# Optimization experiments

Measured on AMD Instinct MI355X. Metric: run time of the kernel, lower is better.

Reference implementation:

```python
import jax, jax.numpy as jnp
import numpy as np

N = 100000
E = 1600000
IN_C = 128
OUT_C = 64
ALPHA = 0.2  # LeakyReLU negative slope


def _xavier(key, shape, gain=1.414):
    fan_in, fan_out = shape[-2] if len(shape) > 1 else shape[-1], shape[-1]
    bound = gain * np.sqrt(6.0 / (shape[0] * 0 + (shape[-2] if len(shape) > 1 else 1) + shape[-1])) if False else gain * np.sqrt(6.0 / (sum(shape)))
    return jax.random.uniform(key, shape, jnp.float32, -bound, bound)


def setup_inputs() -> dict:
    key = jax.random.key(0)
    k_x, k_s, k_o, k_w, k_a = jax.random.split(key, 5)
    x = jax.random.normal(k_x, (N, IN_C), jnp.float32)
    # edge list with no self-loops (so remove_self_loops is a no-op)
    src = jax.random.randint(k_s, (E,), 0, N)
    off = jax.random.randint(k_o, (E,), 1, N)
    dst = (src + off) % N
    edge_index = jnp.stack([src, dst]).astype(jnp.int64)
    W = _xavier(k_w, (IN_C, OUT_C))
    a = _xavier(k_a, (1, 2 * OUT_C))
    return {"x": x, "W": W, "a": a, "edge_index": edge_index}


def reference(x, W, a, edge_index):
    h = x @ W                               # [N, D]
    n, d = h.shape
    loops = jnp.arange(n, dtype=edge_index.dtype)
    src = jnp.concatenate([edge_index[0], loops])   # add_self_loops
    dst = jnp.concatenate([edge_index[1], loops])
    # (cat(h[src], h[dst]) * a).sum(-1) == h[src]@a1 + h[dst]@a2
    a1, a2 = a[0, :d], a[0, d:]
    s = h @ a1                              # [N]
    t = h @ a2                              # [N]
    edge_e = jnp.exp(jax.nn.leaky_relu(s[src] + t[dst], negative_slope=ALPHA))  # [E+N]
    e_expsum = jax.ops.segment_sum(edge_e, src, num_segments=n)                  # [N]
    h_prime = jax.ops.segment_sum(edge_e[:, None] * h[dst], src, num_segments=n)  # [N, D]
    return h_prime / e_expsum[:, None]
```

## Files before the change

### kernel.cpp

```cpp
#include <hip/hip_runtime.h>
#include <math.h>

#define IN_C 128
#define OUT_C 64
#define ALPHA 0.2f

#define LDK 136

#define BSH 7
#define NPB 128
#define MAXB 1024
#define PA_EPT 4
#define PA_THREADS 1024
#define PA_TILE (PA_THREADS * PA_EPT)
#define CHUNK 4096

typedef __attribute__((ext_vector_type(8))) short short8;
typedef __attribute__((ext_vector_type(4))) float v4f;

__device__ __forceinline__ ushort f2b(float f) {
  unsigned u = __float_as_uint(f);
  u += 0x7fffu + ((u >> 16) & 1u);
  return (ushort)(u >> 16);
}

__global__ __launch_bounds__(256) void gemm_st_kernel(
    const float* __restrict__ x, const float* __restrict__ W,
    const float* __restrict__ a, ushort* __restrict__ hb,
    float* __restrict__ s, float* __restrict__ t, int* __restrict__ gcur,
    int nbuck, int cape, int n_nodes, int n_tiles) {
  __shared__ ushort xs[64 * LDK];
  __shared__ ushort ws[64 * LDK];

  const int tid = threadIdx.x;
  const int wave = tid >> 6;
  const int lane = tid & 63;
  const int li = lane & 15;
  const int quad = lane >> 4;

  if (blockIdx.x == 0) {
    for (int i = tid; i < nbuck; i += 256) gcur[i] = i * cape;
  }

  for (int i = tid; i < IN_C * OUT_C; i += 256) {
    const int k = i >> 6;
    const int n = i & 63;
    ws[n * LDK + k] = f2b(W[i]);
  }
  __syncthreads();

  short8 bfrag[4][4];
#pragma unroll
  for (int ct = 0; ct < 4; ++ct)
#pragma unroll
    for (int kk = 0; kk < 4; ++kk)
      bfrag[ct][kk] =
          *(const short8*)&ws[(ct * 16 + li) * LDK + kk * 32 + quad * 8];

  float a1v[4], a2v[4];
#pragma unroll
  for (int ct = 0; ct < 4; ++ct) {
    a1v[ct] = a[ct * 16 + li];
    a2v[ct] = a[OUT_C + ct * 16 + li];
  }

  for (int tile = blockIdx.x; tile < n_tiles; tile += gridDim.x) {
    const int row0 = tile * 64;

    __syncthreads();
    for (int i = tid; i < 64 * (IN_C / 4); i += 256) {
      const int r = i >> 5;
      const int c4 = i & 31;
      int row = row0 + r;
      row = row < n_nodes ? row : n_nodes - 1;
      const float4 v = *(const float4*)&x[(size_t)row * IN_C + c4 * 4];
      uint2 p;
      p.x = (unsigned)f2b(v.x) | ((unsigned)f2b(v.y) << 16);
      p.y = (unsigned)f2b(v.z) | ((unsigned)f2b(v.w) << 16);
      *(uint2*)&xs[r * LDK + c4 * 4] = p;
    }
    __syncthreads();

    v4f acc[4];
#pragma unroll
    for (int ct = 0; ct < 4; ++ct) acc[ct] = (v4f){0.f, 0.f, 0.f, 0.f};

    const int rbase = wave * 16;
#pragma unroll
    for (int kk = 0; kk < 4; ++kk) {
      const short8 af =
          *(const short8*)&xs[(rbase + li) * LDK + kk * 32 + quad * 8];
#pragma unroll
      for (int ct = 0; ct < 4; ++ct)
        acc[ct] = __builtin_amdgcn_mfma_f32_16x16x32_bf16(af, bfrag[ct][kk],
                                                          acc[ct], 0, 0, 0);
    }

    float ps[4] = {0.f, 0.f, 0.f, 0.f};
    float pt[4] = {0.f, 0.f, 0.f, 0.f};
#pragma unroll
    for (int ct = 0; ct < 4; ++ct) {
#pragma unroll
      for (int r = 0; r < 4; ++r) {
        const float hv = acc[ct][r];
        ps[r] += hv * a1v[ct];
        pt[r] += hv * a2v[ct];
      }
    }
#pragma unroll
    for (int m = 1; m <= 8; m <<= 1) {
#pragma unroll
      for (int r = 0; r < 4; ++r) {
        ps[r] += __shfl_xor(ps[r], m, 64);
        pt[r] += __shfl_xor(pt[r], m, 64);
      }
    }
    const int growbase = row0 + rbase + quad * 4;
    if (li < 4) {
      const int grow = growbase + li;
      if (grow < n_nodes) {
        const float sv = li == 0 ? ps[0] : li == 1 ? ps[1] : li == 2 ? ps[2] : ps[3];
        const float tv = li == 0 ? pt[0] : li == 1 ? pt[1] : li == 2 ? pt[2] : pt[3];
        s[grow] = sv;
        t[grow] = tv;
      }
    }

    __syncthreads();
#pragma unroll
    for (int ct = 0; ct < 4; ++ct)
#pragma unroll
      for (int r = 0; r < 4; ++r)
        xs[(rbase + quad * 4 + r) * LDK + ct * 16 + li] = f2b(acc[ct][r]);
    __syncthreads();
    for (int j = tid; j < 64 * 8; j += 256) {
      const int row = j >> 3;
      const int u8 = j & 7;
      const int grow = row0 + row;
      if (grow < n_nodes) {
        const uint4 v = *(const uint4*)&xs[row * LDK + u8 * 8];
        *(uint4*)&hb[(size_t)grow * OUT_C + u8 * 8] = v;
      }
    }
  }
}

__global__ __launch_bounds__(PA_THREADS) void pa_bin(
    const int* __restrict__ src, const int* __restrict__ dst,
    int* __restrict__ gcur, int* __restrict__ pairs, int nbuck, int cape,
    int E) {
  __shared__ int hist[MAXB];
  __shared__ int loffs[MAXB];
  __shared__ int lcur[MAXB];
  __shared__ int gbase[MAXB];
  __shared__ int wsum[16];
  __shared__ int sl[PA_TILE];
  __shared__ ushort sbkt[PA_TILE];

  const int tid = threadIdx.x;
  const int lane = tid & 63;
  const int wid = tid >> 6;
  hist[tid] = 0;
  __syncthreads();

  const int eblk0 = blockIdx.x * PA_TILE;
  const int nblk_edges = min(PA_TILE, E - eblk0);
  const int e0 = eblk0 + tid * PA_EPT;

  int4 sv, dv;
  const bool full = (e0 + PA_EPT <= E);
  if (full) {
    sv = *(const int4*)(src + e0);
    dv = *(const int4*)(dst + e0);
    atomicAdd(&hist[sv.x >> BSH], 1);
    atomicAdd(&hist[sv.y >> BSH], 1);
    atomicAdd(&hist[sv.z >> BSH], 1);
    atomicAdd(&hist[sv.w >> BSH], 1);
  } else {
    for (int e = e0; e < E; ++e) atomicAdd(&hist[src[e] >> BSH], 1);
  }
  __syncthreads();

  const int c = hist[tid];
  gbase[tid] = c ? atomicAdd(&gcur[tid], c) : 0;

  int incl = c;
#pragma unroll
  for (int off = 1; off < 64; off <<= 1) {
    const int o = __shfl_up(incl, off, 64);
    if (lane >= off) incl += o;
  }
  if (lane == 63) wsum[wid] = incl;
  __syncthreads();
  if (tid < 16) {
    const int v = wsum[tid];
    int sc = v;
#pragma unroll
    for (int off = 1; off < 16; off <<= 1) {
      const int o = __shfl_up(sc, off, 64);
      if (tid >= off) sc += o;
    }
    wsum[tid] = sc - v;
  }
  __syncthreads();
  const int excl = incl - c + wsum[wid];
  loffs[tid] = excl;
  lcur[tid] = excl;
  __syncthreads();

#define PUTS(svv, dvv)                                        \
  {                                                           \
    const int bkt = (svv) >> BSH;                             \
    const int pos = atomicAdd(&lcur[bkt], 1);                 \
    sl[pos] = (((svv) & (NPB - 1)) << 25) | (dvv);            \
    sbkt[pos] = (ushort)bkt;                                  \
  }
  if (full) {
    PUTS(sv.x, dv.x);
    PUTS(sv.y, dv.y);
    PUTS(sv.z, dv.z);
    PUTS(sv.w, dv.w);
  } else {
    for (int e = e0; e < E; ++e) {
      const int svv = src[e];
      const int dvv = dst[e];
      PUTS(svv, dvv);
    }
  }
#undef PUTS
  __syncthreads();

  for (int k = tid; k < nblk_edges; k += PA_THREADS) {
    const int bkt = sbkt[k];
    const int gpos = gbase[bkt] + (k - loffs[bkt]);
    if (gpos < (bkt + 1) * cape) pairs[gpos] = sl[k];
  }
}

#define ACC8(o, p, wgt)                                      \
  acc[(o) + 0] += (wgt)*__uint_as_float((p).x << 16);        \
  acc[(o) + 1] += (wgt)*__uint_as_float((p).x & 0xffff0000u);\
  acc[(o) + 2] += (wgt)*__uint_as_float((p).y << 16);        \
  acc[(o) + 3] += (wgt)*__uint_as_float((p).y & 0xffff0000u);\
  acc[(o) + 4] += (wgt)*__uint_as_float((p).z << 16);        \
  acc[(o) + 5] += (wgt)*__uint_as_float((p).z & 0xffff0000u);\
  acc[(o) + 6] += (wgt)*__uint_as_float((p).w << 16);        \
  acc[(o) + 7] += (wgt)*__uint_as_float((p).w & 0xffff0000u);

__global__ __launch_bounds__(256) void aggregate_sorted(
    const int* __restrict__ pairs, const int* __restrict__ gcur,
    const uint4* __restrict__ hb4, const float* __restrict__ s,
    const float* __restrict__ t, float* __restrict__ out, int n_nodes,
    int cape) {
  __shared__ int sl[CHUNK];
  __shared__ int cnt[NPB];
  __shared__ int loffs[NPB];
  __shared__ int cur[NPB];
  __shared__ int w0tot_sh;

  const int b = blockIdx.x;
  const int tid = threadIdx.x;
  const int base = b * cape;
  int fill = gcur[b] - base;
  fill = fill < cape ? fill : cape;

  const int local = tid >> 1;
  const int half = tid & 1;
  const int u = b * NPB + local;
  const bool valid = u < n_nodes;
  const float su = valid ? s[u] : 0.f;

  float acc[32];
#pragma unroll
  for (int i = 0; i < 32; ++i) acc[i] = 0.f;
  float den = 0.f;

  for (int c0 = 0; c0 < fill; c0 += CHUNK) {
    const int clen = min(CHUNK, fill - c0);
    if (tid < NPB) cnt[tid] = 0;
    __syncthreads();

    int pw[CHUNK / 256];
#pragma unroll
    for (int j = 0; j < CHUNK / 256; ++j) {
      const int k = j * 256 + tid;
      if (k < clen) {
        pw[j] = pairs[base + c0 + k];
        atomicAdd(&cnt[((unsigned)pw[j]) >> 25], 1);
      }
    }
    __syncthreads();

    int c = 0, incl = 0;
    if (tid < NPB) {
      c = cnt[tid];
      incl = c;
#pragma unroll
      for (int off = 1; off < 64; off <<= 1) {
        const int o = __shfl_up(incl, off, 64);
        if ((tid & 63) >= off) incl += o;
      }
      if (tid == 63) w0tot_sh = incl;
    }
    __syncthreads();
    if (tid < NPB) {
      if (tid >= 64) incl += w0tot_sh;
      loffs[tid] = incl - c;
      cur[tid] = incl - c;
    }
    __syncthreads();

#pragma unroll
    for (int j = 0; j < CHUNK / 256; ++j) {
      const int k = j * 256 + tid;
      if (k < clen) {
        const int lo = ((unsigned)pw[j]) >> 25;
        const int pos = atomicAdd(&cur[lo], 1);
        sl[pos] = pw[j] & 0x1ffffff;
      }
    }
    __syncthreads();

    const int s0 = loffs[local];
    const int s1 = s0 + cnt[local];
    int e = s0;
    for (; e + 1 < s1; e += 2) {
      const int va = sl[e];
      const int vb = sl[e + 1];
      const float ta = t[va];
      const float tb = t[vb];
      const uint4* ra = &hb4[(size_t)va * 8 + half * 4];
      const uint4* rb = &hb4[(size_t)vb * 8 + half * 4];
      const uint4 pa0 = ra[0], pa1 = ra[1], pa2 = ra[2], pa3 = ra[3];
      const uint4 pb0 = rb[0], pb1 = rb[1], pb2 = rb[2], pb3 = rb[3];
      float za = su + ta;
      float zb = su + tb;
      za = za > 0.f ? za : ALPHA * za;
      zb = zb > 0.f ? zb : ALPHA * zb;
      const float wa = __expf(za);
      const float wb = __expf(zb);
      ACC8(0, pa0, wa) ACC8(8, pa1, wa) ACC8(16, pa2, wa) ACC8(24, pa3, wa)
      ACC8(0, pb0, wb) ACC8(8, pb1, wb) ACC8(16, pb2, wb) ACC8(24, pb3, wb)
      den += wa + wb;
    }
    if (e < s1) {
      const int va = sl[e];
      const float ta = t[va];
      const uint4* ra = &hb4[(size_t)va * 8 + half * 4];
      const uint4 pa0 = ra[0], pa1 = ra[1], pa2 = ra[2], pa3 = ra[3];
      float za = su + ta;
      za = za > 0.f ? za : ALPHA * za;
      const float wa = __expf(za);
      ACC8(0, pa0, wa) ACC8(8, pa1, wa) ACC8(16, pa2, wa) ACC8(24, pa3, wa)
      den += wa;
    }
    __syncthreads();
  }

  if (valid) {
    float z0 = su + t[u];
    z0 = z0 > 0.f ? z0 : ALPHA * z0;
    const float w0 = __expf(z0);
    const uint4* rs = &hb4[(size_t)u * 8 + half * 4];
    const uint4 q0 = rs[0], q1 = rs[1], q2 = rs[2], q3 = rs[3];
    ACC8(0, q0, w0) ACC8(8, q1, w0) ACC8(16, q2, w0) ACC8(24, q3, w0)
    den += w0;
    const float inv = 1.f / den;
#pragma unroll
    for (int q = 0; q < 8; ++q) {
      float4 o;
      o.x = acc[q * 4 + 0] * inv;
      o.y = acc[q * 4 + 1] * inv;
      o.z = acc[q * 4 + 2] * inv;
      o.w = acc[q * 4 + 3] * inv;
      *(float4*)&out[(size_t)u * OUT_C + half * 32 + q * 4] = o;
    }
  }
}

extern "C" void kernel_launch(void* const* d_in, const int* in_sizes, int n_in,
                              void* d_out, int out_size, void* d_ws,
                              size_t ws_size, hipStream_t stream) {
  const float* x = (const float*)d_in[0];
  const float* W = (const float*)d_in[1];
  const float* a = (const float*)d_in[2];
  const int* edge_index = (const int*)d_in[3];

  const int n_nodes = in_sizes[0] / IN_C;
  const int E = in_sizes[3] / 2;
  const int* src = edge_index;
  const int* dst = edge_index + E;

  float* out = (float*)d_out;

  const int nbuck = (n_nodes + NPB - 1) >> BSH;
  const int cape = (((E + nbuck - 1) / nbuck) + 768 + 15) & ~15;
  const int nblk_bin = (E + PA_TILE - 1) / PA_TILE;

  ushort* hb = (ushort*)d_ws;
  float* s = (float*)(hb + (size_t)n_nodes * OUT_C);
  float* t = s + n_nodes;
  int* gcur = (int*)(t + n_nodes);
  int* pairs = gcur + MAXB;

  {
    const int n_tiles = (n_nodes + 63) / 64;
    const int ngrid = n_tiles < 512 ? n_tiles : 512;
    gemm_st_kernel<<<ngrid, 256, 0, stream>>>(x, W, a, hb, s, t, gcur, nbuck,
                                              cape, n_nodes, n_tiles);
  }

  pa_bin<<<nblk_bin, PA_THREADS, 0, stream>>>(src, dst, gcur, pairs, nbuck,
                                              cape, E);

  aggregate_sorted<<<nbuck, 256, 0, stream>>>(pairs, gcur, (const uint4*)hb, s,
                                              t, out, n_nodes, cape);
}
```

Measured before the change: 177.1 us.

## Fuse edge binning and GEMM into one kernel with disjoint block roles

Merges the bf16 GEMM/score kernel and the edge-binning kernel into one launch. The first blocks bin edges and the remaining blocks run the GEMM tiles, so the two independent stages run concurrently instead of serially. Bucket fill counters now start at zero through a memset instead of being set inside the GEMM kernel. Binning blocks shrink to 256 threads that each handle 16 edges, with a 4-bucket-per-thread scan. The change adds a memset launch, and shared memory is sized for the larger of the two roles, which may lower occupancy for the GEMM blocks.

Result: slower. 200.4 us (+13.1%).

```diff
diff --git a/kernel.cpp b/kernel.cpp
--- a/kernel.cpp
+++ b/kernel.cpp
@@ -10,10 +10,10 @@
 #define BSH 7
 #define NPB 128
 #define MAXB 1024
-#define PA_EPT 4
-#define PA_THREADS 1024
-#define PA_TILE (PA_THREADS * PA_EPT)
+#define PA_EPT 16
+#define PA_TILE (256 * PA_EPT)
 #define CHUNK 4096
+#define SMEM_BYTES 41216
 
 typedef __attribute__((ext_vector_type(8))) short short8;
 typedef __attribute__((ext_vector_type(4))) float v4f;
@@ -24,23 +24,129 @@
   return (ushort)(u >> 16);
 }
 
-__global__ __launch_bounds__(256) void gemm_st_kernel(
+__global__ __launch_bounds__(256) void fused_prep(
     const float* __restrict__ x, const float* __restrict__ W,
-    const float* __restrict__ a, ushort* __restrict__ hb,
-    float* __restrict__ s, float* __restrict__ t, int* __restrict__ gcur,
-    int nbuck, int cape, int n_nodes, int n_tiles) {
-  __shared__ ushort xs[64 * LDK];
-  __shared__ ushort ws[64 * LDK];
-
+    const float* __restrict__ a, const int* __restrict__ src,
+    const int* __restrict__ dst, ushort* __restrict__ hb,
+    float* __restrict__ s, float* __restrict__ t, int* __restrict__ gfill,
+    int* __restrict__ pairs, int nbuck, int cape, int n_nodes, int n_tiles,
+    int nbin, int E) {
+  __shared__ __align__(16) char smem[SMEM_BYTES];
   const int tid = threadIdx.x;
+
+  if ((int)blockIdx.x < nbin) {
+    int* hist = (int*)smem;
+    int* loffsB = hist + MAXB;
+    int* lcurB = loffsB + MAXB;
+    int* gbaseB = lcurB + MAXB;
+    int* wsumB = gbaseB + MAXB;
+    int* sl = wsumB + 64;
+    ushort* sbkt = (ushort*)(sl + PA_TILE);
+
+    for (int i = tid; i < MAXB; i += 256) hist[i] = 0;
+    __syncthreads();
+
+    const int eblk0 = blockIdx.x * PA_TILE;
+    const int nblk_edges = min(PA_TILE, E - eblk0);
+    const int e0 = eblk0 + tid * PA_EPT;
+    const bool full = (e0 + PA_EPT <= E);
+
+    if (full) {
+#pragma unroll
+      for (int i = 0; i < PA_EPT / 4; ++i) {
+        const int4 v = *(const int4*)(src + e0 + i * 4);
+        atomicAdd(&hist[v.x >> BSH], 1);
+        atomicAdd(&hist[v.y >> BSH], 1);
+        atomicAdd(&hist[v.z >> BSH], 1);
+        atomicAdd(&hist[v.w >> BSH], 1);
+      }
+    } else {
+      for (int e = e0; e < E; ++e) atomicAdd(&hist[src[e] >> BSH], 1);
+    }
+    __syncthreads();
+
+    const int lane = tid & 63;
+    const int wid = tid >> 6;
+    int c4[4], csum = 0;
+#pragma unroll
+    for (int j = 0; j < 4; ++j) {
+      c4[j] = hist[tid * 4 + j];
+      csum += c4[j];
+    }
+    int incl = csum;
+#pragma unroll
+    for (int off = 1; off < 64; off <<= 1) {
+      const int o = __shfl_up(incl, off, 64);
+      if (lane >= off) incl += o;
+    }
+    if (lane == 63) wsumB[wid] = incl;
+    __syncthreads();
+    if (tid == 0) {
+      int r = 0;
+#pragma unroll
+      for (int j = 0; j < 4; ++j) {
+        const int v = wsumB[j];
+        wsumB[4 + j] = r;
+        r += v;
+      }
+    }
+    __syncthreads();
+    int run = incl - csum + wsumB[4 + wid];
+#pragma unroll
+    for (int j = 0; j < 4; ++j) {
+      const int bkt = tid * 4 + j;
+      loffsB[bkt] = run;
+      lcurB[bkt] = run;
+      const int cc = c4[j];
+      gbaseB[bkt] = cc ? atomicAdd(&gfill[bkt], cc) : 0;
+      run += cc;
+    }
+    __syncthreads();
+
+#define PUTS(svv, dvv)                                \
+  {                                                   \
+    const int bkt = (svv) >> BSH;                     \
+    const int pos = atomicAdd(&lcurB[bkt], 1);        \
+    sl[pos] = (((svv) & (NPB - 1)) << 25) | (dvv);    \
+    sbkt[pos] = (ushort)bkt;                          \
+  }
+    if (full) {
+#pragma unroll
+      for (int i = 0; i < PA_EPT / 4; ++i) {
+        const int4 sv = *(const int4*)(src + e0 + i * 4);
+        const int4 dv = *(const int4*)(dst + e0 + i * 4);
+        PUTS(sv.x, dv.x);
+        PUTS(sv.y, dv.y);
+        PUTS(sv.z, dv.z);
+        PUTS(sv.w, dv.w);
+      }
+    } else {
+      for (int e = e0; e < E; ++e) {
+        const int svv = src[e];
+        const int dvv = dst[e];
+        PUTS(svv, dvv);
+      }
+    }
+#undef PUTS
+    __syncthreads();
+
+    for (int k = tid; k < nblk_edges; k += 256) {
+      const int bkt = sbkt[k];
+      const int off = gbaseB[bkt] + (k - loffsB[bkt]);
+      if (off < cape) pairs[bkt * cape + off] = sl[k];
+    }
+    return;
+  }
+
+  ushort* xs = (ushort*)smem;
+  ushort* ws = xs + 64 * LDK;
+
   const int wave = tid >> 6;
   const int lane = tid & 63;
   const int li = lane & 15;
   const int quad = lane >> 4;
-
-  if (blockIdx.x == 0) {
-    for (int i = tid; i < nbuck; i += 256) gcur[i] = i * cape;
-  }
+  const int gblocks = gridDim.x - nbin;
+  const int gbid = blockIdx.x - nbin;
 
   for (int i = tid; i < IN_C * OUT_C; i += 256) {
     const int k = i >> 6;
@@ -64,7 +170,7 @@
     a2v[ct] = a[OUT_C + ct * 16 + li];
   }
 
-  for (int tile = blockIdx.x; tile < n_tiles; tile += gridDim.x) {
+  for (int tile = gbid; tile < n_tiles; tile += gblocks) {
     const int row0 = tile * 64;
 
     __syncthreads();
@@ -145,98 +251,6 @@
   }
 }
 
-__global__ __launch_bounds__(PA_THREADS) void pa_bin(
-    const int* __restrict__ src, const int* __restrict__ dst,
-    int* __restrict__ gcur, int* __restrict__ pairs, int nbuck, int cape,
-    int E) {
-  __shared__ int hist[MAXB];
-  __shared__ int loffs[MAXB];
-  __shared__ int lcur[MAXB];
-  __shared__ int gbase[MAXB];
-  __shared__ int wsum[16];
-  __shared__ int sl[PA_TILE];
-  __shared__ ushort sbkt[PA_TILE];
-
-  const int tid = threadIdx.x;
-  const int lane = tid & 63;
-  const int wid = tid >> 6;
-  hist[tid] = 0;
-  __syncthreads();
-
-  const int eblk0 = blockIdx.x * PA_TILE;
-  const int nblk_edges = min(PA_TILE, E - eblk0);
-  const int e0 = eblk0 + tid * PA_EPT;
-
-  int4 sv, dv;
-  const bool full = (e0 + PA_EPT <= E);
-  if (full) {
-    sv = *(const int4*)(src + e0);
-    dv = *(const int4*)(dst + e0);
-    atomicAdd(&hist[sv.x >> BSH], 1);
-    atomicAdd(&hist[sv.y >> BSH], 1);
-    atomicAdd(&hist[sv.z >> BSH], 1);
-    atomicAdd(&hist[sv.w >> BSH], 1);
-  } else {
-    for (int e = e0; e < E; ++e) atomicAdd(&hist[src[e] >> BSH], 1);
-  }
-  __syncthreads();
-
-  const int c = hist[tid];
-  gbase[tid] = c ? atomicAdd(&gcur[tid], c) : 0;
-
-  int incl = c;
-#pragma unroll
-  for (int off = 1; off < 64; off <<= 1) {
-    const int o = __shfl_up(incl, off, 64);
-    if (lane >= off) incl += o;
-  }
-  if (lane == 63) wsum[wid] = incl;
-  __syncthreads();
-  if (tid < 16) {
-    const int v = wsum[tid];
-    int sc = v;
-#pragma unroll
-    for (int off = 1; off < 16; off <<= 1) {
-      const int o = __shfl_up(sc, off, 64);
-      if (tid >= off) sc += o;
-    }
-    wsum[tid] = sc - v;
-  }
-  __syncthreads();
-  const int excl = incl - c + wsum[wid];
-  loffs[tid] = excl;
-  lcur[tid] = excl;
-  __syncthreads();
-
-#define PUTS(svv, dvv)                                        \
-  {                                                           \
-    const int bkt = (svv) >> BSH;                             \
-    const int pos = atomicAdd(&lcur[bkt], 1);                 \
-    sl[pos] = (((svv) & (NPB - 1)) << 25) | (dvv);            \
-    sbkt[pos] = (ushort)bkt;                                  \
-  }
-  if (full) {
-    PUTS(sv.x, dv.x);
-    PUTS(sv.y, dv.y);
-    PUTS(sv.z, dv.z);
-    PUTS(sv.w, dv.w);
-  } else {
-    for (int e = e0; e < E; ++e) {
-      const int svv = src[e];
-      const int dvv = dst[e];
-      PUTS(svv, dvv);
-    }
-  }
-#undef PUTS
-  __syncthreads();
-
-  for (int k = tid; k < nblk_edges; k += PA_THREADS) {
-    const int bkt = sbkt[k];
-    const int gpos = gbase[bkt] + (k - loffs[bkt]);
-    if (gpos < (bkt + 1) * cape) pairs[gpos] = sl[k];
-  }
-}
-
 #define ACC8(o, p, wgt)                                      \
   acc[(o) + 0] += (wgt)*__uint_as_float((p).x << 16);        \
   acc[(o) + 1] += (wgt)*__uint_as_float((p).x & 0xffff0000u);\
@@ -248,7 +262,7 @@
   acc[(o) + 7] += (wgt)*__uint_as_float((p).w & 0xffff0000u);
 
 __global__ __launch_bounds__(256) void aggregate_sorted(
-    const int* __restrict__ pairs, const int* __restrict__ gcur,
+    const int* __restrict__ pairs, const int* __restrict__ gfill,
     const uint4* __restrict__ hb4, const float* __restrict__ s,
     const float* __restrict__ t, float* __restrict__ out, int n_nodes,
     int cape) {
@@ -261,7 +275,7 @@
   const int b = blockIdx.x;
   const int tid = threadIdx.x;
   const int base = b * cape;
-  int fill = gcur[b] - base;
+  int fill = gfill[b];
   fill = fill < cape ? fill : cape;
 
   const int local = tid >> 1;
@@ -395,24 +409,22 @@
 
   const int nbuck = (n_nodes + NPB - 1) >> BSH;
   const int cape = (((E + nbuck - 1) / nbuck) + 768 + 15) & ~15;
-  const int nblk_bin = (E + PA_TILE - 1) / PA_TILE;
+  const int nbin = (E + PA_TILE - 1) / PA_TILE;
+  const int n_tiles = (n_nodes + 63) / 64;
+  const int ngemm = n_tiles < 512 ? n_tiles : 512;
 
   ushort* hb = (ushort*)d_ws;
   float* s = (float*)(hb + (size_t)n_nodes * OUT_C);
   float* t = s + n_nodes;
-  int* gcur = (int*)(t + n_nodes);
-  int* pairs = gcur + MAXB;
-
-  {
-    const int n_tiles = (n_nodes + 63) / 64;
-    const int ngrid = n_tiles < 512 ? n_tiles : 512;
-    gemm_st_kernel<<<ngrid, 256, 0, stream>>>(x, W, a, hb, s, t, gcur, nbuck,
-                                              cape, n_nodes, n_tiles);
-  }
-
-  pa_bin<<<nblk_bin, PA_THREADS, 0, stream>>>(src, dst, gcur, pairs, nbuck,
-                                              cape, E);
-
-  aggregate_sorted<<<nbuck, 256, 0, stream>>>(pairs, gcur, (const uint4*)hb, s,
-                                              t, out, n_nodes, cape);
+  int* gfill = (int*)(t + n_nodes);
+  int* pairs = gfill + MAXB;
+
+  hipMemsetAsync(gfill, 0, MAXB * sizeof(int), stream);
+
+  fused_prep<<<nbin + ngemm, 256, 0, stream>>>(x, W, a, src, dst, hb, s, t,
+                                               gfill, pairs, nbuck, cape,
+                                               n_nodes, n_tiles, nbin, E);
+
+  aggregate_sorted<<<nbuck, 256, 0, stream>>>(pairs, gfill, (const uint4*)hb,
+                                              s, t, out, n_nodes, cape);
 }
```
